# Optimization experiments

Hardware: AMD Instinct MI355X
Metric: run time of the kernel (lower is better)

The kernel has to match this reference:

```python
import jax, jax.numpy as jnp
import numpy as np

GROUP = 128  # GPTQ group size


def _dequant(qweight, qzeros, scales):
    """Dequantize GPTQ int4 packed weights.
    qweight: [K//8, N] int32, 8 nibbles packed along input dim
    qzeros : [G, N//8] int32, 8 nibbles packed along output dim
    scales : [G, N] float
    returns W: [K, N] float, W[r,n] = scales[g,n] * (q[r,n] - (z[g,n]+1)), g = r//GROUP
    """
    shifts = jnp.arange(8, dtype=jnp.int32) * 4
    K8, N = qweight.shape
    # unpack input-dim nibbles: [K//8, 8, N] -> [K, N]
    wi = ((qweight[:, None, :] >> shifts[None, :, None]) & 0xF).reshape(K8 * 8, N)
    # unpack output-dim nibbles: [G, N//8, 8] -> [G, N]
    G = qzeros.shape[0]
    z = ((qzeros[:, :, None] >> shifts[None, None, :]) & 0xF).reshape(G, N)
    g = jnp.arange(K8 * 8) // GROUP  # group index per input row
    return scales[g] * (wi.astype(scales.dtype) - (z[g].astype(scales.dtype) + 1.0))


def setup_inputs() -> dict:
    key = jax.random.key(0)
    k1, k2, k3, k4, k5 = jax.random.split(key, 5)
    B, S, K, N = 4, 32, 4096, 14336
    G = K // GROUP
    x = jax.random.normal(k1, (B, S, K), dtype=jnp.float32)
    qweight = jax.random.randint(k2, (K // 8, N), 0, 2**31 - 1, dtype=jnp.int32)
    qzeros = jax.random.randint(k3, (G, N // 8), 0, 2**31 - 1, dtype=jnp.int32)
    scales = jax.random.uniform(k4, (G, N), dtype=jnp.float32, minval=0.001, maxval=0.02)
    bias = jax.random.normal(k5, (N,), dtype=jnp.float32) * 0.01
    return {"x": x, "qweight": qweight, "qzeros": qzeros, "scales": scales, "bias": bias}


def reference(x, qweight, qzeros, scales, bias):
    # fused dequant + GEMM: out = x @ dequant(W) + bias, shape [B, S, N]
    W = _dequant(qweight, qzeros, scales)
    return x @ W + bias
```

## Files before the change

kernel.cpp:

```cpp
#include <hip/hip_runtime.h>
#include <hip/hip_fp16.h>

typedef _Float16 half8 __attribute__((ext_vector_type(8)));
typedef _Float16 half2v __attribute__((ext_vector_type(2)));
typedef float f32x16 __attribute__((ext_vector_type(16)));

#define BM 128
#define BN 256
#define BK 64
#define THREADS 512
#define LDS_TILE (BM * BK * 2)

__device__ inline unsigned pkrtz(float lo, float hi) {
  return __builtin_bit_cast(unsigned, __builtin_amdgcn_cvt_pkrtz(lo, hi));
}

#define BAR() do { \
  asm volatile("s_waitcnt lgkmcnt(0)" ::: "memory"); \
  __builtin_amdgcn_s_barrier(); \
} while (0)

__global__ void init_out_kernel(const float* __restrict__ bias,
                                float* __restrict__ out, int MN, int N) {
  int i = (blockIdx.x * blockDim.x + threadIdx.x) * 4;
  if (i < MN) *(float4*)(out + i) = *(const float4*)(bias + (i % N));
}

__global__ void reduce_kernel(const float* __restrict__ ws,
                              const float* __restrict__ bias,
                              float* __restrict__ out, int MN, int N, int S) {
  int i = (blockIdx.x * blockDim.x + threadIdx.x) * 4;
  if (i >= MN) return;
  float4 a = *(const float4*)(bias + (i % N));
  for (int z = 0; z < S; ++z) {
    float4 p = *(const float4*)(ws + (size_t)z * MN + i);
    a.x += p.x; a.y += p.y; a.z += p.z; a.w += p.w;
  }
  *(float4*)(out + i) = a;
}

struct Bs {
  unsigned w0[4], w1[4];
  unsigned zr0, sr0, zr1, sr1;
};

__device__ inline half8 dequant(unsigned w, unsigned zr, unsigned sr) {
  half2v zh = __builtin_bit_cast(half2v, zr);
  half2v sh = __builtin_bit_cast(half2v, sr);
  unsigned u0 = (w & 0x000F000Fu) | 0x64006400u;
  unsigned u1 = ((w >> 4) & 0x000F000Fu) | 0x64006400u;
  unsigned u2 = ((w >> 8) & 0x000F000Fu) | 0x64006400u;
  unsigned u3 = ((w >> 12) & 0x000F000Fu) | 0x64006400u;
  uint4 r;
  r.x = __builtin_bit_cast(unsigned, (half2v)((__builtin_bit_cast(half2v, u0) - zh) * sh));
  r.y = __builtin_bit_cast(unsigned, (half2v)((__builtin_bit_cast(half2v, u1) - zh) * sh));
  r.z = __builtin_bit_cast(unsigned, (half2v)((__builtin_bit_cast(half2v, u2) - zh) * sh));
  r.w = __builtin_bit_cast(unsigned, (half2v)((__builtin_bit_cast(half2v, u3) - zh) * sh));
  return __builtin_bit_cast(half8, r);
}

__global__ __launch_bounds__(THREADS) void qgemm_kernel(
    const float* __restrict__ x, const int* __restrict__ qw,
    const int* __restrict__ qz, const float* __restrict__ sc,
    float* __restrict__ target, int N, int K, int S, int use_ws) {
  __shared__ __align__(16) unsigned char smem[2 * LDS_TILE];
  const int tid = threadIdx.x;
  const int n0 = blockIdx.x * BN;
  const int z = blockIdx.z;
  const int KC = K / S;
  const int kbase = z * KC;
  const int nt = KC / BK;
  const int lane = tid & 63;
  const int wid = tid >> 6;
  const int wr = wid >> 2;
  const int wc = wid & 3;
  const int l31 = lane & 31;
  const int l5 = lane >> 5;
  const int N8 = N >> 3;
  const int kqb = kbase >> 3;

  f32x16 acc[2][2] = {};

  const int arow = tid >> 2;
  const int aq = tid & 3;
  const int c0 = n0 + wc * 64 + l31;
  const int c1 = c0 + 32;

  float4 areg[4];
  auto LOADA = [&](int t) {
    const float* src = x + arow * K + kbase + t * BK + aq * 16;
#pragma unroll
    for (int j = 0; j < 4; ++j) areg[j] = *(const float4*)(src + 4 * j);
  };

  auto STOREA = [&](int buf) {
    unsigned char* base = smem + buf * LDS_TILE;
#pragma unroll
    for (int j = 0; j < 2; ++j) {
      uint4 q;
      q.x = pkrtz(areg[2 * j].x, areg[2 * j + 1].x);
      q.y = pkrtz(areg[2 * j].y, areg[2 * j + 1].y);
      q.z = pkrtz(areg[2 * j].z, areg[2 * j + 1].z);
      q.w = pkrtz(areg[2 * j].w, areg[2 * j + 1].w);
      int u = aq * 2 + j;
      *(uint4*)(base + arow * 128 + ((u ^ (arow & 7)) << 4)) = q;
    }
  };

  auto LOADB = [&](int t, Bs& b) {
    const int* q0 = qw + (kqb + t * 8 + l5) * N + c0;
#pragma unroll
    for (int s = 0; s < 4; ++s) {
      b.w0[s] = (unsigned)q0[2 * s * N];
      b.w1[s] = (unsigned)q0[2 * s * N + 32];
    }
    int g = (kbase + t * BK) >> 7;
    int zw0 = qz[g * N8 + (c0 >> 3)];
    int zw1 = qz[g * N8 + (c1 >> 3)];
    b.zr0 = (0x6401u + (unsigned)((zw0 >> ((c0 & 7) * 4)) & 0xF)) * 0x00010001u;
    b.zr1 = (0x6401u + (unsigned)((zw1 >> ((c1 & 7) * 4)) & 0xF)) * 0x00010001u;
    float s0 = sc[g * N + c0], s1 = sc[g * N + c1];
    b.sr0 = pkrtz(s0, s0);
    b.sr1 = pkrtz(s1, s1);
  };

  auto COMPUTE = [&](int buf, const Bs& b) {
    unsigned char* base = smem + buf * LDS_TILE;
#pragma unroll
    for (int s = 0; s < 4; ++s) {
      int u = 2 * s + l5;
      half8 a0, a1, b0, b1;
      {
        int row = wr * 64 + l31;
        a0 = *(half8*)(base + row * 128 + ((u ^ (row & 7)) << 4));
        row += 32;
        a1 = *(half8*)(base + row * 128 + ((u ^ (row & 7)) << 4));
      }
      b0 = dequant(b.w0[s], b.zr0, b.sr0);
      b1 = dequant(b.w1[s], b.zr1, b.sr1);
      acc[0][0] = __builtin_amdgcn_mfma_f32_32x32x16_f16(a0, b0, acc[0][0], 0, 0, 0);
      acc[0][1] = __builtin_amdgcn_mfma_f32_32x32x16_f16(a0, b1, acc[0][1], 0, 0, 0);
      acc[1][0] = __builtin_amdgcn_mfma_f32_32x32x16_f16(a1, b0, acc[1][0], 0, 0, 0);
      acc[1][1] = __builtin_amdgcn_mfma_f32_32x32x16_f16(a1, b1, acc[1][1], 0, 0, 0);
    }
  };

  Bs b0, b1;
  LOADA(0);
  LOADB(0, b0);
  STOREA(0);
  LOADA(1);
  LOADB(1, b1);
  __syncthreads();

  for (int t = 0; t < nt; t += 2) {
    STOREA(1);
    { int tn = t + 2 < nt ? t + 2 : nt - 1; LOADA(tn); }
    COMPUTE(0, b0);
    { int tn = t + 2 < nt ? t + 2 : nt - 1; LOADB(tn, b0); }
    BAR();

    STOREA(0);
    { int tn = t + 3 < nt ? t + 3 : nt - 1; LOADA(tn); }
    COMPUTE(1, b1);
    { int tn = t + 3 < nt ? t + 3 : nt - 1; LOADB(tn, b1); }
    BAR();
  }

  if (use_ws) {
    float* o = target + (size_t)z * (size_t)BM * N;
#pragma unroll
    for (int fi = 0; fi < 2; ++fi)
#pragma unroll
      for (int fj = 0; fj < 2; ++fj) {
        int gc = n0 + wc * 64 + fj * 32 + l31;
#pragma unroll
        for (int r = 0; r < 16; ++r) {
          int gm = wr * 64 + fi * 32 + (r & 3) + 8 * (r >> 2) + 4 * l5;
          o[(size_t)gm * N + gc] = acc[fi][fj][r];
        }
      }
  } else {
#pragma unroll
    for (int fi = 0; fi < 2; ++fi)
#pragma unroll
      for (int fj = 0; fj < 2; ++fj) {
        int gc = n0 + wc * 64 + fj * 32 + l31;
#pragma unroll
        for (int r = 0; r < 16; ++r) {
          int gm = wr * 64 + fi * 32 + (r & 3) + 8 * (r >> 2) + 4 * l5;
          unsafeAtomicAdd(&target[(size_t)gm * N + gc], acc[fi][fj][r]);
        }
      }
  }
}

extern "C" void kernel_launch(void* const* d_in, const int* in_sizes, int n_in,
                              void* d_out, int out_size, void* d_ws, size_t ws_size,
                              hipStream_t stream) {
  const float* x = (const float*)d_in[0];
  const int* qw = (const int*)d_in[1];
  const int* qz = (const int*)d_in[2];
  const float* sc = (const float*)d_in[3];
  const float* bias = (const float*)d_in[4];
  float* out = (float*)d_out;

  int N = in_sizes[4];
  int K = (in_sizes[1] / N) * 8;
  int M = in_sizes[0] / K;
  int MN = M * N;
  size_t slice = (size_t)MN * 4;

  int S = 0;
  if (ws_size >= 8 * slice) S = 8;
  else if (ws_size >= 4 * slice) S = 4;
  else if (ws_size >= 2 * slice) S = 2;

  if (S > 0) {
    dim3 grid(N / BN, 1, S);
    qgemm_kernel<<<grid, THREADS, 0, stream>>>(x, qw, qz, sc, (float*)d_ws,
                                               N, K, S, 1);
    reduce_kernel<<<(MN / 4 + 255) / 256, 256, 0, stream>>>(
        (const float*)d_ws, bias, out, MN, N, S);
  } else {
    init_out_kernel<<<(MN / 4 + 255) / 256, 256, 0, stream>>>(bias, out, MN, N);
    dim3 grid(N / BN, 1, 8);
    qgemm_kernel<<<grid, THREADS, 0, stream>>>(x, qw, qz, sc, out, N, K, 8, 0);
  }
}
```

Measured before the change: 48.68 us.

## Shrink N tile to 64 with 256 threads and template the K-tile count

The output-column tile drops from 256 to 64 and the block from 512 to 256 threads, so each wave now computes one 32-column fragment over 64 rows. The grid becomes four times larger, which should fill the MI355X CUs better for this skinny M=128 GEMM. The number of K tiles becomes a template parameter so the main loop can be fully unrolled. The trade-off is that each block reloads and converts the whole 128-row A slice for a quarter as many columns, which raises A traffic and reuse overhead, and each wave gets less MFMA work per LDS read.

```diff
diff --git a/kernel.cpp b/kernel.cpp
--- a/kernel.cpp
+++ b/kernel.cpp
@@ -6,9 +6,9 @@
 typedef float f32x16 __attribute__((ext_vector_type(16)));
 
 #define BM 128
-#define BN 256
+#define BN 64
 #define BK 64
-#define THREADS 512
+#define THREADS 256
 #define LDS_TILE (BM * BK * 2)
 
 __device__ inline unsigned pkrtz(float lo, float hi) {
@@ -40,8 +40,8 @@
 }
 
 struct Bs {
-  unsigned w0[4], w1[4];
-  unsigned zr0, sr0, zr1, sr1;
+  unsigned w[4];
+  unsigned zr, sr;
 };
 
 __device__ inline half8 dequant(unsigned w, unsigned zr, unsigned sr) {
@@ -59,50 +59,49 @@
   return __builtin_bit_cast(half8, r);
 }
 
+template <int NT>
 __global__ __launch_bounds__(THREADS) void qgemm_kernel(
     const float* __restrict__ x, const int* __restrict__ qw,
     const int* __restrict__ qz, const float* __restrict__ sc,
-    float* __restrict__ target, int N, int K, int S, int use_ws) {
+    float* __restrict__ target, int N, int K, int use_ws) {
   __shared__ __align__(16) unsigned char smem[2 * LDS_TILE];
   const int tid = threadIdx.x;
   const int n0 = blockIdx.x * BN;
   const int z = blockIdx.z;
-  const int KC = K / S;
+  const int KC = NT * BK;
   const int kbase = z * KC;
-  const int nt = KC / BK;
   const int lane = tid & 63;
   const int wid = tid >> 6;
-  const int wr = wid >> 2;
-  const int wc = wid & 3;
+  const int wr = wid >> 1;
+  const int wc = wid & 1;
   const int l31 = lane & 31;
   const int l5 = lane >> 5;
   const int N8 = N >> 3;
   const int kqb = kbase >> 3;
 
-  f32x16 acc[2][2] = {};
-
-  const int arow = tid >> 2;
-  const int aq = tid & 3;
-  const int c0 = n0 + wc * 64 + l31;
-  const int c1 = c0 + 32;
-
-  float4 areg[4];
+  f32x16 acc0 = {}, acc1 = {};
+
+  const int arow = tid >> 1;
+  const int ah = tid & 1;
+  const int c0 = n0 + wc * 32 + l31;
+
+  float4 areg[8];
   auto LOADA = [&](int t) {
-    const float* src = x + arow * K + kbase + t * BK + aq * 16;
-#pragma unroll
-    for (int j = 0; j < 4; ++j) areg[j] = *(const float4*)(src + 4 * j);
+    const float* src = x + arow * K + kbase + t * BK + ah * 32;
+#pragma unroll
+    for (int j = 0; j < 8; ++j) areg[j] = *(const float4*)(src + 4 * j);
   };
 
   auto STOREA = [&](int buf) {
     unsigned char* base = smem + buf * LDS_TILE;
 #pragma unroll
-    for (int j = 0; j < 2; ++j) {
+    for (int j = 0; j < 4; ++j) {
       uint4 q;
       q.x = pkrtz(areg[2 * j].x, areg[2 * j + 1].x);
       q.y = pkrtz(areg[2 * j].y, areg[2 * j + 1].y);
       q.z = pkrtz(areg[2 * j].z, areg[2 * j + 1].z);
       q.w = pkrtz(areg[2 * j].w, areg[2 * j + 1].w);
-      int u = aq * 2 + j;
+      int u = ah * 4 + j;
       *(uint4*)(base + arow * 128 + ((u ^ (arow & 7)) << 4)) = q;
     }
   };
@@ -110,18 +109,12 @@
   auto LOADB = [&](int t, Bs& b) {
     const int* q0 = qw + (kqb + t * 8 + l5) * N + c0;
 #pragma unroll
-    for (int s = 0; s < 4; ++s) {
-      b.w0[s] = (unsigned)q0[2 * s * N];
-      b.w1[s] = (unsigned)q0[2 * s * N + 32];
-    }
+    for (int s = 0; s < 4; ++s) b.w[s] = (unsigned)q0[2 * s * N];
     int g = (kbase + t * BK) >> 7;
-    int zw0 = qz[g * N8 + (c0 >> 3)];
-    int zw1 = qz[g * N8 + (c1 >> 3)];
-    b.zr0 = (0x6401u + (unsigned)((zw0 >> ((c0 & 7) * 4)) & 0xF)) * 0x00010001u;
-    b.zr1 = (0x6401u + (unsigned)((zw1 >> ((c1 & 7) * 4)) & 0xF)) * 0x00010001u;
-    float s0 = sc[g * N + c0], s1 = sc[g * N + c1];
-    b.sr0 = pkrtz(s0, s0);
-    b.sr1 = pkrtz(s1, s1);
+    int zw = qz[g * N8 + (c0 >> 3)];
+    b.zr = (0x6401u + (unsigned)((zw >> ((c0 & 7) * 4)) & 0xF)) * 0x00010001u;
+    float s0 = sc[g * N + c0];
+    b.sr = pkrtz(s0, s0);
   };
 
   auto COMPUTE = [&](int buf, const Bs& b) {
@@ -129,19 +122,13 @@
 #pragma unroll
     for (int s = 0; s < 4; ++s) {
       int u = 2 * s + l5;
-      half8 a0, a1, b0, b1;
-      {
-        int row = wr * 64 + l31;
-        a0 = *(half8*)(base + row * 128 + ((u ^ (row & 7)) << 4));
-        row += 32;
-        a1 = *(half8*)(base + row * 128 + ((u ^ (row & 7)) << 4));
-      }
-      b0 = dequant(b.w0[s], b.zr0, b.sr0);
-      b1 = dequant(b.w1[s], b.zr1, b.sr1);
-      acc[0][0] = __builtin_amdgcn_mfma_f32_32x32x16_f16(a0, b0, acc[0][0], 0, 0, 0);
-      acc[0][1] = __builtin_amdgcn_mfma_f32_32x32x16_f16(a0, b1, acc[0][1], 0, 0, 0);
-      acc[1][0] = __builtin_amdgcn_mfma_f32_32x32x16_f16(a1, b0, acc[1][0], 0, 0, 0);
-      acc[1][1] = __builtin_amdgcn_mfma_f32_32x32x16_f16(a1, b1, acc[1][1], 0, 0, 0);
+      int row0 = wr * 64 + l31;
+      half8 a0 = *(half8*)(base + row0 * 128 + ((u ^ (row0 & 7)) << 4));
+      int row1 = row0 + 32;
+      half8 a1 = *(half8*)(base + row1 * 128 + ((u ^ (row1 & 7)) << 4));
+      half8 bf = dequant(b.w[s], b.zr, b.sr);
+      acc0 = __builtin_amdgcn_mfma_f32_32x32x16_f16(a0, bf, acc0, 0, 0, 0);
+      acc1 = __builtin_amdgcn_mfma_f32_32x32x16_f16(a1, bf, acc1, 0, 0, 0);
     }
   };
 
@@ -153,45 +140,36 @@
   LOADB(1, b1);
   __syncthreads();
 
-  for (int t = 0; t < nt; t += 2) {
+#pragma unroll
+  for (int t = 0; t < NT; t += 2) {
     STOREA(1);
-    { int tn = t + 2 < nt ? t + 2 : nt - 1; LOADA(tn); }
+    { int tn = t + 2 < NT ? t + 2 : NT - 1; LOADA(tn); }
     COMPUTE(0, b0);
-    { int tn = t + 2 < nt ? t + 2 : nt - 1; LOADB(tn, b0); }
+    { int tn = t + 2 < NT ? t + 2 : NT - 1; LOADB(tn, b0); }
     BAR();
 
     STOREA(0);
-    { int tn = t + 3 < nt ? t + 3 : nt - 1; LOADA(tn); }
+    { int tn = t + 3 < NT ? t + 3 : NT - 1; LOADA(tn); }
     COMPUTE(1, b1);
-    { int tn = t + 3 < nt ? t + 3 : nt - 1; LOADB(tn, b1); }
+    { int tn = t + 3 < NT ? t + 3 : NT - 1; LOADB(tn, b1); }
     BAR();
   }
 
   if (use_ws) {
     float* o = target + (size_t)z * (size_t)BM * N;
 #pragma unroll
-    for (int fi = 0; fi < 2; ++fi)
-#pragma unroll
-      for (int fj = 0; fj < 2; ++fj) {
-        int gc = n0 + wc * 64 + fj * 32 + l31;
-#pragma unroll
-        for (int r = 0; r < 16; ++r) {
-          int gm = wr * 64 + fi * 32 + (r & 3) + 8 * (r >> 2) + 4 * l5;
-          o[(size_t)gm * N + gc] = acc[fi][fj][r];
-        }
-      }
+    for (int r = 0; r < 16; ++r) {
+      int gm = wr * 64 + (r & 3) + 8 * (r >> 2) + 4 * l5;
+      o[(size_t)gm * N + c0] = acc0[r];
+      o[(size_t)(gm + 32) * N + c0] = acc1[r];
+    }
   } else {
 #pragma unroll
-    for (int fi = 0; fi < 2; ++fi)
-#pragma unroll
-      for (int fj = 0; fj < 2; ++fj) {
-        int gc = n0 + wc * 64 + fj * 32 + l31;
-#pragma unroll
-        for (int r = 0; r < 16; ++r) {
-          int gm = wr * 64 + fi * 32 + (r & 3) + 8 * (r >> 2) + 4 * l5;
-          unsafeAtomicAdd(&target[(size_t)gm * N + gc], acc[fi][fj][r]);
-        }
-      }
+    for (int r = 0; r < 16; ++r) {
+      int gm = wr * 64 + (r & 3) + 8 * (r >> 2) + 4 * l5;
+      unsafeAtomicAdd(&target[(size_t)gm * N + c0], acc0[r]);
+      unsafeAtomicAdd(&target[(size_t)(gm + 32) * N + c0], acc1[r]);
+    }
   }
 }
 
@@ -216,15 +194,24 @@
   else if (ws_size >= 4 * slice) S = 4;
   else if (ws_size >= 2 * slice) S = 2;
 
-  if (S > 0) {
-    dim3 grid(N / BN, 1, S);
-    qgemm_kernel<<<grid, THREADS, 0, stream>>>(x, qw, qz, sc, (float*)d_ws,
-                                               N, K, S, 1);
+  if (S == 8) {
+    dim3 grid(N / BN, 1, 8);
+    qgemm_kernel<8><<<grid, THREADS, 0, stream>>>(x, qw, qz, sc, (float*)d_ws, N, K, 1);
     reduce_kernel<<<(MN / 4 + 255) / 256, 256, 0, stream>>>(
-        (const float*)d_ws, bias, out, MN, N, S);
+        (const float*)d_ws, bias, out, MN, N, 8);
+  } else if (S == 4) {
+    dim3 grid(N / BN, 1, 4);
+    qgemm_kernel<16><<<grid, THREADS, 0, stream>>>(x, qw, qz, sc, (float*)d_ws, N, K, 1);
+    reduce_kernel<<<(MN / 4 + 255) / 256, 256, 0, stream>>>(
+        (const float*)d_ws, bias, out, MN, N, 4);
+  } else if (S == 2) {
+    dim3 grid(N / BN, 1, 2);
+    qgemm_kernel<32><<<grid, THREADS, 0, stream>>>(x, qw, qz, sc, (float*)d_ws, N, K, 1);
+    reduce_kernel<<<(MN / 4 + 255) / 256, 256, 0, stream>>>(
+        (const float*)d_ws, bias, out, MN, N, 2);
   } else {
     init_out_kernel<<<(MN / 4 + 255) / 256, 256, 0, stream>>>(bias, out, MN, N);
     dim3 grid(N / BN, 1, 8);
-    qgemm_kernel<<<grid, THREADS, 0, stream>>>(x, qw, qz, sc, out, N, K, 8, 0);
-  }
-}
+    qgemm_kernel<8><<<grid, THREADS, 0, stream>>>(x, qw, qz, sc, out, N, K, 0);
+  }
+}
```

After: 84.05 us. +72.6%, slower.
